# Performance work log

Measured on AMD Instinct MI355X. Metric: run time of the kernel, lower is better.

Reference implementation:

```python
import jax, jax.numpy as jnp
import numpy as np

N, K, F_IN, F_OUT, P = 50000, 32, 64, 64, 3


def setup_inputs() -> dict:
    key = jax.random.key(0)
    k1, k2, k3, k4, k5 = jax.random.split(key, 5)
    h = jax.random.normal(k1, (N, F_IN), dtype=jnp.float32)
    pos = jax.random.normal(k2, (N, P), dtype=jnp.float32)
    neighbor_idx = jax.random.randint(k3, (N, K), 0, N, dtype=jnp.int32)
    weight = jax.random.normal(k4, (K * F_IN, F_OUT), dtype=jnp.float32) * 0.02
    bias_p = jax.random.normal(k5, (1, F_OUT), dtype=jnp.float32) * 0.02
    return {"h": h, "pos": pos, "neighbor_idx": neighbor_idx,
            "weight": weight, "bias_p": bias_p}


def reference(h, pos, neighbor_idx, weight, bias_p):
    n, k = neighbor_idx.shape
    msgs = h[neighbor_idx]                      # [N, K, F_IN] gather
    diff = pos[:, None, :] - pos[neighbor_idx]  # [N, K, P]
    sq = jnp.sum(diff * diff, axis=2, keepdims=True)  # [N, K, 1]
    # torch: dist[dist==0] = 0.5 ; safe-sqrt avoids NaN grads at 0
    dist = jnp.where(sq == 0.0, 0.5, jnp.sqrt(jnp.where(sq == 0.0, 1.0, sq)))
    wow = (msgs / dist).reshape(n, k * h.shape[1])  # [N, K*F_IN]
    h1 = wow @ weight + bias_p                   # [N, F_OUT]
    return jax.nn.leaky_relu(h1, negative_slope=0.01)
```

## Files before the change

kernel.cpp:

```cpp
#include <hip/hip_runtime.h>


#define N_NODES 50000
#define KN      32
#define FIN     64
#define FOUT    64
#define MTILE   64

typedef __attribute__((ext_vector_type(4))) float    f32x4;
typedef __attribute__((ext_vector_type(8))) _Float16 f16x8;
typedef __attribute__((ext_vector_type(4))) _Float16 f16x4;

__global__ void k_conv_h(const float* __restrict__ src, _Float16* __restrict__ dst) {
    int i = blockIdx.x * blockDim.x + threadIdx.x;
    float4 v = ((const float4*)src)[i];
    f16x4 o = { (_Float16)v.x, (_Float16)v.y, (_Float16)v.z, (_Float16)v.w };
    ((f16x4*)dst)[i] = o;
}

__global__ void k_conv_w(const float* __restrict__ w, _Float16* __restrict__ wf) {
    __shared__ float s_w[32 * 64];
    const int kk = blockIdx.x, tid = threadIdx.x;
    for (int p = tid; p < 32 * 64; p += 256)
        s_w[p] = w[kk * 32 * 64 + p];
    __syncthreads();
    const int t = tid >> 6, lane = tid & 63;
    const int lm = lane & 15, q = lane >> 4;
    f16x8 o;
    #pragma unroll
    for (int i = 0; i < 8; ++i)
        o[i] = (_Float16)s_w[(q * 8 + i) * 64 + t * 16 + lm];
    *(f16x8*)(wf + (((kk * 4 + t) * 64) + lane) * 8) = o;
}

__global__ __launch_bounds__(256, 3) void k_main(
        const _Float16* __restrict__ hf,
        const float*    __restrict__ pos,
        const int*      __restrict__ nidx,
        const _Float16* __restrict__ wf,
        const float*    __restrict__ bias,
        float*          __restrict__ out)
{
    __shared__ int2  s_e[KN * MTILE];
    __shared__ float s_red[2 * 64 * 68];

    const int tid = threadIdx.x;
    const int m0  = blockIdx.x * MTILE;

    for (int p = tid; p < MTILE * KN; p += 256) {
        int m = p & 63, k = p >> 6;
        int node = m0 + m;
        int idx = 0; float scl = 0.f;
        if (node < N_NODES) {
            idx = nidx[node * KN + k];
            float dx = pos[node * 3 + 0] - pos[idx * 3 + 0];
            float dy = pos[node * 3 + 1] - pos[idx * 3 + 1];
            float dz = pos[node * 3 + 2] - pos[idx * 3 + 2];
            float sq = dx * dx + dy * dy + dz * dz;
            scl = (sq == 0.f) ? 2.0f : rsqrtf(sq);
        }
        s_e[k * MTILE + m] = make_int2(idx, __float_as_int(scl));
    }
    __syncthreads();

    const int lane = tid & 63, wv = tid >> 6;
    const int lm = lane & 15, q = lane >> 4;

    const _Float16* pb = wf + wv * 32768 + lane * 8;

    f32x4 acc[4][4] = {};

    #pragma unroll 2
    for (int knl = 0; knl < 8; ++knl) {
        const int kb = (wv * 8 + knl) * MTILE + lm;
        const int2 e0 = s_e[kb];
        const int2 e1 = s_e[kb + 16];
        const int2 e2 = s_e[kb + 32];
        const int2 e3 = s_e[kb + 48];
        const _Float16* pa0 = hf + e0.x * FIN + q * 8;
        const _Float16* pa1 = hf + e1.x * FIN + q * 8;
        const _Float16* pa2 = hf + e2.x * FIN + q * 8;
        const _Float16* pa3 = hf + e3.x * FIN + q * 8;
        const _Float16 s0 = (_Float16)__int_as_float(e0.y);
        const _Float16 s1 = (_Float16)__int_as_float(e1.y);
        const _Float16 s2 = (_Float16)__int_as_float(e2.y);
        const _Float16 s3 = (_Float16)__int_as_float(e3.y);
        #pragma unroll
        for (int jh = 0; jh < 2; ++jh) {
            const int fo = ((knl * 2 + jh) * 4) * 512;
            f16x8 b0 = *(const f16x8*)(pb + fo);
            f16x8 b1 = *(const f16x8*)(pb + fo + 512);
            f16x8 b2 = *(const f16x8*)(pb + fo + 1024);
            f16x8 b3 = *(const f16x8*)(pb + fo + 1536);
            f16x8 a0 = *(const f16x8*)(pa0 + jh * 32) * s0;
            f16x8 a1 = *(const f16x8*)(pa1 + jh * 32) * s1;
            f16x8 a2 = *(const f16x8*)(pa2 + jh * 32) * s2;
            f16x8 a3 = *(const f16x8*)(pa3 + jh * 32) * s3;
            acc[0][0] = __builtin_amdgcn_mfma_f32_16x16x32_f16(a0, b0, acc[0][0], 0, 0, 0);
            acc[0][1] = __builtin_amdgcn_mfma_f32_16x16x32_f16(a0, b1, acc[0][1], 0, 0, 0);
            acc[0][2] = __builtin_amdgcn_mfma_f32_16x16x32_f16(a0, b2, acc[0][2], 0, 0, 0);
            acc[0][3] = __builtin_amdgcn_mfma_f32_16x16x32_f16(a0, b3, acc[0][3], 0, 0, 0);
            acc[1][0] = __builtin_amdgcn_mfma_f32_16x16x32_f16(a1, b0, acc[1][0], 0, 0, 0);
            acc[1][1] = __builtin_amdgcn_mfma_f32_16x16x32_f16(a1, b1, acc[1][1], 0, 0, 0);
            acc[1][2] = __builtin_amdgcn_mfma_f32_16x16x32_f16(a1, b2, acc[1][2], 0, 0, 0);
            acc[1][3] = __builtin_amdgcn_mfma_f32_16x16x32_f16(a1, b3, acc[1][3], 0, 0, 0);
            acc[2][0] = __builtin_amdgcn_mfma_f32_16x16x32_f16(a2, b0, acc[2][0], 0, 0, 0);
            acc[2][1] = __builtin_amdgcn_mfma_f32_16x16x32_f16(a2, b1, acc[2][1], 0, 0, 0);
            acc[2][2] = __builtin_amdgcn_mfma_f32_16x16x32_f16(a2, b2, acc[2][2], 0, 0, 0);
            acc[2][3] = __builtin_amdgcn_mfma_f32_16x16x32_f16(a2, b3, acc[2][3], 0, 0, 0);
            acc[3][0] = __builtin_amdgcn_mfma_f32_16x16x32_f16(a3, b0, acc[3][0], 0, 0, 0);
            acc[3][1] = __builtin_amdgcn_mfma_f32_16x16x32_f16(a3, b1, acc[3][1], 0, 0, 0);
            acc[3][2] = __builtin_amdgcn_mfma_f32_16x16x32_f16(a3, b2, acc[3][2], 0, 0, 0);
            acc[3][3] = __builtin_amdgcn_mfma_f32_16x16x32_f16(a3, b3, acc[3][3], 0, 0, 0);
        }
    }

    float* reg = s_red + (wv & 1) * (64 * 68);
    if (wv < 2) {
        #pragma unroll
        for (int mt = 0; mt < 4; ++mt)
            #pragma unroll
            for (int t = 0; t < 4; ++t)
                #pragma unroll
                for (int r = 0; r < 4; ++r)
                    reg[(mt * 16 + q * 4 + r) * 68 + t * 16 + lm] = acc[mt][t][r];
    }
    __syncthreads();
    if (wv >= 2) {
        #pragma unroll
        for (int mt = 0; mt < 4; ++mt)
            #pragma unroll
            for (int t = 0; t < 4; ++t)
                #pragma unroll
                for (int r = 0; r < 4; ++r)
                    reg[(mt * 16 + q * 4 + r) * 68 + t * 16 + lm] += acc[mt][t][r];
    }
    __syncthreads();

    const int row = tid >> 2, c0 = (tid & 3) * 16;
    const int node = m0 + row;
    if (node < N_NODES) {
        #pragma unroll
        for (int i = 0; i < 4; ++i) {
            int c = c0 + i * 4;
            f32x4 v0 = *(const f32x4*)(s_red + row * 68 + c);
            f32x4 v1 = *(const f32x4*)(s_red + 64 * 68 + row * 68 + c);
            f32x4 bb = *(const f32x4*)(bias + c);
            f32x4 o = v0 + v1 + bb;
            #pragma unroll
            for (int j = 0; j < 4; ++j) o[j] = o[j] > 0.f ? o[j] : 0.01f * o[j];
            *(f32x4*)(out + node * FOUT + c) = o;
        }
    }
}

extern "C" void kernel_launch(void* const* d_in, const int* in_sizes, int n_in,
                              void* d_out, int out_size, void* d_ws, size_t ws_size,
                              hipStream_t stream) {
    const float* h    = (const float*)d_in[0];
    const float* pos  = (const float*)d_in[1];
    const int*   nidx = (const int*)d_in[2];
    const float* w    = (const float*)d_in[3];
    const float* bias = (const float*)d_in[4];
    float* out = (float*)d_out;

    _Float16* wf = (_Float16*)d_ws;
    _Float16* hb = (_Float16*)((char*)d_ws + 262144);

    k_conv_w<<<64, 256, 0, stream>>>(w, wf);
    k_conv_h<<<(N_NODES * FIN / 4) / 256, 256, 0, stream>>>(h, hb);
    k_main<<<(N_NODES + MTILE - 1) / MTILE, 256, 0, stream>>>(hb, pos, nidx, wf, bias, out);
}
```

Measured before the change: 138.0 us.

## Split main tile across 8 waves, prefetch gathered rows, fuse prep kernels

Doubles the main kernel block to 512 threads so each wave handles 32 rows by 4 neighbor groups instead of 64 rows, halving per-wave accumulators. Gathered h rows for the next neighbor are software-prefetched into registers while MFMAs run on the current ones, aiming to hide gather latency. The two preprocessing kernels are merged into one launch to cut launch overhead. Weight fragments are now loaded twice per block (once per row group), adding some L2 traffic, and the reduction still sums only two partial buffers.

After: 136.1 us. About the same (-1.4%).

```diff
diff --git a/kernel.cpp b/kernel.cpp
--- a/kernel.cpp
+++ b/kernel.cpp
@@ -11,29 +11,31 @@
 typedef __attribute__((ext_vector_type(8))) _Float16 f16x8;
 typedef __attribute__((ext_vector_type(4))) _Float16 f16x4;
 
-__global__ void k_conv_h(const float* __restrict__ src, _Float16* __restrict__ dst) {
-    int i = blockIdx.x * blockDim.x + threadIdx.x;
-    float4 v = ((const float4*)src)[i];
-    f16x4 o = { (_Float16)v.x, (_Float16)v.y, (_Float16)v.z, (_Float16)v.w };
-    ((f16x4*)dst)[i] = o;
+__global__ void k_prep(const float* __restrict__ w, _Float16* __restrict__ wf,
+                       const float* __restrict__ h, _Float16* __restrict__ hb) {
+    __shared__ float s_w[32 * 64];
+    const int tid = threadIdx.x;
+    if (blockIdx.x < 64) {
+        const int kk = blockIdx.x;
+        for (int p = tid; p < 32 * 64; p += 256)
+            s_w[p] = w[kk * 32 * 64 + p];
+        __syncthreads();
+        const int t = tid >> 6, lane = tid & 63;
+        const int lm = lane & 15, q = lane >> 4;
+        f16x8 o;
+        #pragma unroll
+        for (int i = 0; i < 8; ++i)
+            o[i] = (_Float16)s_w[(q * 8 + i) * 64 + t * 16 + lm];
+        *(f16x8*)(wf + kk * 2048 + t * 512 + lane * 8) = o;
+    } else {
+        const int i = (blockIdx.x - 64) * 256 + tid;
+        float4 v = ((const float4*)h)[i];
+        f16x4 o = { (_Float16)v.x, (_Float16)v.y, (_Float16)v.z, (_Float16)v.w };
+        ((f16x4*)hb)[i] = o;
+    }
 }
 
-__global__ void k_conv_w(const float* __restrict__ w, _Float16* __restrict__ wf) {
-    __shared__ float s_w[32 * 64];
-    const int kk = blockIdx.x, tid = threadIdx.x;
-    for (int p = tid; p < 32 * 64; p += 256)
-        s_w[p] = w[kk * 32 * 64 + p];
-    __syncthreads();
-    const int t = tid >> 6, lane = tid & 63;
-    const int lm = lane & 15, q = lane >> 4;
-    f16x8 o;
-    #pragma unroll
-    for (int i = 0; i < 8; ++i)
-        o[i] = (_Float16)s_w[(q * 8 + i) * 64 + t * 16 + lm];
-    *(f16x8*)(wf + (((kk * 4 + t) * 64) + lane) * 8) = o;
-}
-
-__global__ __launch_bounds__(256, 3) void k_main(
+__global__ __launch_bounds__(512, 6) void k_main(
         const _Float16* __restrict__ hf,
         const float*    __restrict__ pos,
         const int*      __restrict__ nidx,
@@ -47,7 +49,7 @@
     const int tid = threadIdx.x;
     const int m0  = blockIdx.x * MTILE;
 
-    for (int p = tid; p < MTILE * KN; p += 256) {
+    for (int p = tid; p < MTILE * KN; p += 512) {
         int m = p & 63, k = p >> 6;
         int node = m0 + m;
         int idx = 0; float scl = 0.f;
@@ -65,37 +67,44 @@
 
     const int lane = tid & 63, wv = tid >> 6;
     const int lm = lane & 15, q = lane >> 4;
+    const int mg = wv & 1;
+    const int kg = wv >> 1;
 
-    const _Float16* pb = wf + wv * 32768 + lane * 8;
+    const _Float16* pb = wf + lane * 8;
+    const int ebase = (kg * 8) * MTILE + mg * 32 + lm;
 
-    f32x4 acc[4][4] = {};
+    f32x4 acc[2][4] = {};
 
-    #pragma unroll 2
+    int2 e0 = s_e[ebase], e1 = s_e[ebase + 16];
+    const _Float16* pa0 = hf + e0.x * FIN + q * 8;
+    const _Float16* pa1 = hf + e1.x * FIN + q * 8;
+    f16x8 A00 = *(const f16x8*)pa0, A01 = *(const f16x8*)(pa0 + 32);
+    f16x8 A10 = *(const f16x8*)pa1, A11 = *(const f16x8*)(pa1 + 32);
+    _Float16 s0 = (_Float16)__int_as_float(e0.y);
+    _Float16 s1 = (_Float16)__int_as_float(e1.y);
+
+    #pragma unroll
     for (int knl = 0; knl < 8; ++knl) {
-        const int kb = (wv * 8 + knl) * MTILE + lm;
-        const int2 e0 = s_e[kb];
-        const int2 e1 = s_e[kb + 16];
-        const int2 e2 = s_e[kb + 32];
-        const int2 e3 = s_e[kb + 48];
-        const _Float16* pa0 = hf + e0.x * FIN + q * 8;
-        const _Float16* pa1 = hf + e1.x * FIN + q * 8;
-        const _Float16* pa2 = hf + e2.x * FIN + q * 8;
-        const _Float16* pa3 = hf + e3.x * FIN + q * 8;
-        const _Float16 s0 = (_Float16)__int_as_float(e0.y);
-        const _Float16 s1 = (_Float16)__int_as_float(e1.y);
-        const _Float16 s2 = (_Float16)__int_as_float(e2.y);
-        const _Float16 s3 = (_Float16)__int_as_float(e3.y);
-        #pragma unroll
-        for (int jh = 0; jh < 2; ++jh) {
-            const int fo = ((knl * 2 + jh) * 4) * 512;
-            f16x8 b0 = *(const f16x8*)(pb + fo);
-            f16x8 b1 = *(const f16x8*)(pb + fo + 512);
-            f16x8 b2 = *(const f16x8*)(pb + fo + 1024);
-            f16x8 b3 = *(const f16x8*)(pb + fo + 1536);
-            f16x8 a0 = *(const f16x8*)(pa0 + jh * 32) * s0;
-            f16x8 a1 = *(const f16x8*)(pa1 + jh * 32) * s1;
-            f16x8 a2 = *(const f16x8*)(pa2 + jh * 32) * s2;
-            f16x8 a3 = *(const f16x8*)(pa3 + jh * 32) * s3;
+        f16x8 N00, N01, N10, N11;
+        _Float16 ns0, ns1;
+        if (knl < 7) {
+            int eb = ebase + (knl + 1) * MTILE;
+            int2 f0 = s_e[eb], f1 = s_e[eb + 16];
+            const _Float16* q0 = hf + f0.x * FIN + q * 8;
+            const _Float16* q1 = hf + f1.x * FIN + q * 8;
+            N00 = *(const f16x8*)q0; N01 = *(const f16x8*)(q0 + 32);
+            N10 = *(const f16x8*)q1; N11 = *(const f16x8*)(q1 + 32);
+            ns0 = (_Float16)__int_as_float(f0.y);
+            ns1 = (_Float16)__int_as_float(f1.y);
+        }
+
+        const _Float16* pbb = pb + ((kg * 8 + knl) * 2) * 2048;
+        {
+            f16x8 a0 = A00 * s0, a1 = A10 * s1;
+            f16x8 b0 = *(const f16x8*)(pbb);
+            f16x8 b1 = *(const f16x8*)(pbb + 512);
+            f16x8 b2 = *(const f16x8*)(pbb + 1024);
+            f16x8 b3 = *(const f16x8*)(pbb + 1536);
             acc[0][0] = __builtin_amdgcn_mfma_f32_16x16x32_f16(a0, b0, acc[0][0], 0, 0, 0);
             acc[0][1] = __builtin_amdgcn_mfma_f32_16x16x32_f16(a0, b1, acc[0][1], 0, 0, 0);
             acc[0][2] = __builtin_amdgcn_mfma_f32_16x16x32_f16(a0, b2, acc[0][2], 0, 0, 0);
@@ -104,44 +113,55 @@
             acc[1][1] = __builtin_amdgcn_mfma_f32_16x16x32_f16(a1, b1, acc[1][1], 0, 0, 0);
             acc[1][2] = __builtin_amdgcn_mfma_f32_16x16x32_f16(a1, b2, acc[1][2], 0, 0, 0);
             acc[1][3] = __builtin_amdgcn_mfma_f32_16x16x32_f16(a1, b3, acc[1][3], 0, 0, 0);
-            acc[2][0] = __builtin_amdgcn_mfma_f32_16x16x32_f16(a2, b0, acc[2][0], 0, 0, 0);
-            acc[2][1] = __builtin_amdgcn_mfma_f32_16x16x32_f16(a2, b1, acc[2][1], 0, 0, 0);
-            acc[2][2] = __builtin_amdgcn_mfma_f32_16x16x32_f16(a2, b2, acc[2][2], 0, 0, 0);
-            acc[2][3] = __builtin_amdgcn_mfma_f32_16x16x32_f16(a2, b3, acc[2][3], 0, 0, 0);
-            acc[3][0] = __builtin_amdgcn_mfma_f32_16x16x32_f16(a3, b0, acc[3][0], 0, 0, 0);
-            acc[3][1] = __builtin_amdgcn_mfma_f32_16x16x32_f16(a3, b1, acc[3][1], 0, 0, 0);
-            acc[3][2] = __builtin_amdgcn_mfma_f32_16x16x32_f16(a3, b2, acc[3][2], 0, 0, 0);
-            acc[3][3] = __builtin_amdgcn_mfma_f32_16x16x32_f16(a3, b3, acc[3][3], 0, 0, 0);
+        }
+        {
+            f16x8 a0 = A01 * s0, a1 = A11 * s1;
+            f16x8 b0 = *(const f16x8*)(pbb + 2048);
+            f16x8 b1 = *(const f16x8*)(pbb + 2560);
+            f16x8 b2 = *(const f16x8*)(pbb + 3072);
+            f16x8 b3 = *(const f16x8*)(pbb + 3584);
+            acc[0][0] = __builtin_amdgcn_mfma_f32_16x16x32_f16(a0, b0, acc[0][0], 0, 0, 0);
+            acc[0][1] = __builtin_amdgcn_mfma_f32_16x16x32_f16(a0, b1, acc[0][1], 0, 0, 0);
+            acc[0][2] = __builtin_amdgcn_mfma_f32_16x16x32_f16(a0, b2, acc[0][2], 0, 0, 0);
+            acc[0][3] = __builtin_amdgcn_mfma_f32_16x16x32_f16(a0, b3, acc[0][3], 0, 0, 0);
+            acc[1][0] = __builtin_amdgcn_mfma_f32_16x16x32_f16(a1, b0, acc[1][0], 0, 0, 0);
+            acc[1][1] = __builtin_amdgcn_mfma_f32_16x16x32_f16(a1, b1, acc[1][1], 0, 0, 0);
+            acc[1][2] = __builtin_amdgcn_mfma_f32_16x16x32_f16(a1, b2, acc[1][2], 0, 0, 0);
+            acc[1][3] = __builtin_amdgcn_mfma_f32_16x16x32_f16(a1, b3, acc[1][3], 0, 0, 0);
+        }
+        if (knl < 7) {
+            A00 = N00; A01 = N01; A10 = N10; A11 = N11;
+            s0 = ns0; s1 = ns1;
         }
     }
 
-    float* reg = s_red + (wv & 1) * (64 * 68);
-    if (wv < 2) {
+    float* reg = s_red + (kg & 1) * (64 * 68);
+    if (kg < 2) {
         #pragma unroll
-        for (int mt = 0; mt < 4; ++mt)
+        for (int mt = 0; mt < 2; ++mt)
             #pragma unroll
             for (int t = 0; t < 4; ++t)
                 #pragma unroll
                 for (int r = 0; r < 4; ++r)
-                    reg[(mt * 16 + q * 4 + r) * 68 + t * 16 + lm] = acc[mt][t][r];
+                    reg[(mg * 32 + mt * 16 + q * 4 + r) * 68 + t * 16 + lm] = acc[mt][t][r];
     }
     __syncthreads();
-    if (wv >= 2) {
+    if (kg >= 2) {
         #pragma unroll
-        for (int mt = 0; mt < 4; ++mt)
+        for (int mt = 0; mt < 2; ++mt)
             #pragma unroll
             for (int t = 0; t < 4; ++t)
                 #pragma unroll
                 for (int r = 0; r < 4; ++r)
-                    reg[(mt * 16 + q * 4 + r) * 68 + t * 16 + lm] += acc[mt][t][r];
+                    reg[(mg * 32 + mt * 16 + q * 4 + r) * 68 + t * 16 + lm] += acc[mt][t][r];
     }
     __syncthreads();
 
-    const int row = tid >> 2, c0 = (tid & 3) * 16;
+    const int row = tid >> 3, c0 = (tid & 7) * 8;
     const int node = m0 + row;
     if (node < N_NODES) {
         #pragma unroll
-        for (int i = 0; i < 4; ++i) {
+        for (int i = 0; i < 2; ++i) {
             int c = c0 + i * 4;
             f32x4 v0 = *(const f32x4*)(s_red + row * 68 + c);
             f32x4 v1 = *(const f32x4*)(s_red + 64 * 68 + row * 68 + c);
@@ -167,7 +187,6 @@
     _Float16* wf = (_Float16*)d_ws;
     _Float16* hb = (_Float16*)((char*)d_ws + 262144);
 
-    k_conv_w<<<64, 256, 0, stream>>>(w, wf);
-    k_conv_h<<<(N_NODES * FIN / 4) / 256, 256, 0, stream>>>(h, hb);
-    k_main<<<(N_NODES + MTILE - 1) / MTILE, 256, 0, stream>>>(hb, pos, nidx, wf, bias, out);
+    k_prep<<<64 + (N_NODES * FIN / 4) / 256, 256, 0, stream>>>(w, wf, h, hb);
+    k_main<<<(N_NODES + MTILE - 1) / MTILE, 512, 0, stream>>>(hb, pos, nidx, wf, bias, out);
 }
```

## Merge prep kernels, alias edge and reduction LDS, raise occupancy to four

Applied to the files above, without the earlier changes.

Fuses the weight and h conversion kernels into a single launch, which removes one kernel launch. In the main kernel the edge table and the reduction buffer now share one LDS allocation, with an added barrier between their uses. Launch bounds go from 3 to 4 blocks per CU and the k-loop is no longer unrolled. Together these aim at more waves in flight to hide gather latency, at the cost of tighter register pressure and less instruction-level parallelism per wave.

After: 128.9 us. -6.6%, faster.

```diff
diff --git a/kernel.cpp b/kernel.cpp
--- a/kernel.cpp
+++ b/kernel.cpp
@@ -11,29 +11,31 @@
 typedef __attribute__((ext_vector_type(8))) _Float16 f16x8;
 typedef __attribute__((ext_vector_type(4))) _Float16 f16x4;
 
-__global__ void k_conv_h(const float* __restrict__ src, _Float16* __restrict__ dst) {
-    int i = blockIdx.x * blockDim.x + threadIdx.x;
-    float4 v = ((const float4*)src)[i];
-    f16x4 o = { (_Float16)v.x, (_Float16)v.y, (_Float16)v.z, (_Float16)v.w };
-    ((f16x4*)dst)[i] = o;
+__global__ void k_prep(const float* __restrict__ w, _Float16* __restrict__ wf,
+                       const float* __restrict__ h, _Float16* __restrict__ hb) {
+    __shared__ float s_w[32 * 64];
+    const int tid = threadIdx.x;
+    if (blockIdx.x < 64) {
+        const int kk = blockIdx.x;
+        for (int p = tid; p < 32 * 64; p += 256)
+            s_w[p] = w[kk * 32 * 64 + p];
+        __syncthreads();
+        const int t = tid >> 6, lane = tid & 63;
+        const int lm = lane & 15, q = lane >> 4;
+        f16x8 o;
+        #pragma unroll
+        for (int i = 0; i < 8; ++i)
+            o[i] = (_Float16)s_w[(q * 8 + i) * 64 + t * 16 + lm];
+        *(f16x8*)(wf + kk * 2048 + t * 512 + lane * 8) = o;
+    } else {
+        const int i = (blockIdx.x - 64) * 256 + tid;
+        float4 v = ((const float4*)h)[i];
+        f16x4 o = { (_Float16)v.x, (_Float16)v.y, (_Float16)v.z, (_Float16)v.w };
+        ((f16x4*)hb)[i] = o;
+    }
 }
 
-__global__ void k_conv_w(const float* __restrict__ w, _Float16* __restrict__ wf) {
-    __shared__ float s_w[32 * 64];
-    const int kk = blockIdx.x, tid = threadIdx.x;
-    for (int p = tid; p < 32 * 64; p += 256)
-        s_w[p] = w[kk * 32 * 64 + p];
-    __syncthreads();
-    const int t = tid >> 6, lane = tid & 63;
-    const int lm = lane & 15, q = lane >> 4;
-    f16x8 o;
-    #pragma unroll
-    for (int i = 0; i < 8; ++i)
-        o[i] = (_Float16)s_w[(q * 8 + i) * 64 + t * 16 + lm];
-    *(f16x8*)(wf + (((kk * 4 + t) * 64) + lane) * 8) = o;
-}
-
-__global__ __launch_bounds__(256, 3) void k_main(
+__global__ __launch_bounds__(256, 4) void k_main(
         const _Float16* __restrict__ hf,
         const float*    __restrict__ pos,
         const int*      __restrict__ nidx,
@@ -41,8 +43,9 @@
         const float*    __restrict__ bias,
         float*          __restrict__ out)
 {
-    __shared__ int2  s_e[KN * MTILE];
-    __shared__ float s_red[2 * 64 * 68];
+    __shared__ __align__(16) char smem[2 * 64 * 68 * 4];
+    int2*  s_e   = (int2*)smem;
+    float* s_red = (float*)smem;
 
     const int tid = threadIdx.x;
     const int m0  = blockIdx.x * MTILE;
@@ -63,20 +66,20 @@
     }
     __syncthreads();
 
-    const int lane = tid & 63, wv = tid >> 6;
+    const int lane = tid & 63, kg = tid >> 6;
     const int lm = lane & 15, q = lane >> 4;
 
-    const _Float16* pb = wf + wv * 32768 + lane * 8;
+    const _Float16* pb = wf + lane * 8;
 
     f32x4 acc[4][4] = {};
 
-    #pragma unroll 2
-    for (int knl = 0; knl < 8; ++knl) {
-        const int kb = (wv * 8 + knl) * MTILE + lm;
-        const int2 e0 = s_e[kb];
-        const int2 e1 = s_e[kb + 16];
-        const int2 e2 = s_e[kb + 32];
-        const int2 e3 = s_e[kb + 48];
+    #pragma unroll 1
+    for (int j = 0; j < 8; ++j) {
+        const int kn = kg * 8 + j;
+        int2 e0 = s_e[kn * MTILE + lm];
+        int2 e1 = s_e[kn * MTILE + 16 + lm];
+        int2 e2 = s_e[kn * MTILE + 32 + lm];
+        int2 e3 = s_e[kn * MTILE + 48 + lm];
         const _Float16* pa0 = hf + e0.x * FIN + q * 8;
         const _Float16* pa1 = hf + e1.x * FIN + q * 8;
         const _Float16* pa2 = hf + e2.x * FIN + q * 8;
@@ -85,13 +88,14 @@
         const _Float16 s1 = (_Float16)__int_as_float(e1.y);
         const _Float16 s2 = (_Float16)__int_as_float(e2.y);
         const _Float16 s3 = (_Float16)__int_as_float(e3.y);
+
         #pragma unroll
         for (int jh = 0; jh < 2; ++jh) {
-            const int fo = ((knl * 2 + jh) * 4) * 512;
-            f16x8 b0 = *(const f16x8*)(pb + fo);
-            f16x8 b1 = *(const f16x8*)(pb + fo + 512);
-            f16x8 b2 = *(const f16x8*)(pb + fo + 1024);
-            f16x8 b3 = *(const f16x8*)(pb + fo + 1536);
+            const _Float16* pbb = pb + (kn * 2 + jh) * 2048;
+            f16x8 b0 = *(const f16x8*)(pbb);
+            f16x8 b1 = *(const f16x8*)(pbb + 512);
+            f16x8 b2 = *(const f16x8*)(pbb + 1024);
+            f16x8 b3 = *(const f16x8*)(pbb + 1536);
             f16x8 a0 = *(const f16x8*)(pa0 + jh * 32) * s0;
             f16x8 a1 = *(const f16x8*)(pa1 + jh * 32) * s1;
             f16x8 a2 = *(const f16x8*)(pa2 + jh * 32) * s2;
@@ -115,8 +119,10 @@
         }
     }
 
-    float* reg = s_red + (wv & 1) * (64 * 68);
-    if (wv < 2) {
+    __syncthreads();
+
+    float* reg = s_red + (kg & 1) * (64 * 68);
+    if (kg < 2) {
         #pragma unroll
         for (int mt = 0; mt < 4; ++mt)
             #pragma unroll
@@ -126,7 +132,7 @@
                     reg[(mt * 16 + q * 4 + r) * 68 + t * 16 + lm] = acc[mt][t][r];
     }
     __syncthreads();
-    if (wv >= 2) {
+    if (kg >= 2) {
         #pragma unroll
         for (int mt = 0; mt < 4; ++mt)
             #pragma unroll
@@ -148,7 +154,7 @@
             f32x4 bb = *(const f32x4*)(bias + c);
             f32x4 o = v0 + v1 + bb;
             #pragma unroll
-            for (int j = 0; j < 4; ++j) o[j] = o[j] > 0.f ? o[j] : 0.01f * o[j];
+            for (int jj = 0; jj < 4; ++jj) o[jj] = o[jj] > 0.f ? o[jj] : 0.01f * o[jj];
             *(f32x4*)(out + node * FOUT + c) = o;
         }
     }
@@ -167,7 +173,6 @@
     _Float16* wf = (_Float16*)d_ws;
     _Float16* hb = (_Float16*)((char*)d_ws + 262144);
 
-    k_conv_w<<<64, 256, 0, stream>>>(w, wf);
-    k_conv_h<<<(N_NODES * FIN / 4) / 256, 256, 0, stream>>>(h, hb);
+    k_prep<<<64 + (N_NODES * FIN / 4) / 256, 256, 0, stream>>>(w, wf, h, hb);
     k_main<<<(N_NODES + MTILE - 1) / MTILE, 256, 0, stream>>>(hb, pos, nidx, wf, bias, out);
 }
```
